# Optimization experiments

Measured on AMD Instinct MI355X. Metric: run time of the kernel, lower is better.

## Reference

```python
import jax, jax.numpy as jnp
import numpy as np

NUM_HEADS = 12
HEAD_DIM = 64
HIDDEN = NUM_HEADS * HEAD_DIM  # 768


def setup_inputs() -> dict:
    key = jax.random.key(0)
    ks = jax.random.split(key, 18)
    B, Ni, Nt, H = 8, 1024, 512, HIDDEN
    inp = {
        "hidden_states": jax.random.normal(ks[0], (B, Ni, H), jnp.float32),
        "text": jax.random.normal(ks[1], (B, Nt, H), jnp.float32),
    }
    names = ["Wq", "Wk", "Wv", "Wqt", "Wkt", "Wvt", "Wo"]
    for i, n in enumerate(names):
        inp[n] = jax.random.normal(ks[2 + i], (H, H), jnp.float32) * 0.02
        inp["b" + n[1:]] = jnp.zeros((H,), jnp.float32)
    return inp


def _split_heads(x):
    # [B, S, H] -> [B, h, S, dh]
    B, S, _ = x.shape
    return x.reshape(B, S, NUM_HEADS, HEAD_DIM).transpose(0, 2, 1, 3)


def _merge_heads(x):
    # [B, h, S, dh] -> [B, S, H]
    B, h, S, dh = x.shape
    return x.transpose(0, 2, 1, 3).reshape(B, S, h * dh)


def _attend(q, k, v):
    scale = 1.0 / jnp.sqrt(jnp.asarray(HEAD_DIM, q.dtype))
    scores = jnp.einsum("bhqd,bhkd->bhqk", q, k) * scale
    probs = jax.nn.softmax(scores, axis=-1)
    ctx = jnp.einsum("bhqk,bhkd->bhqd", probs, v)
    return ctx, probs


def reference(hidden_states, text, Wq, bq, Wk, bk, Wv, bv,
              Wqt, bqt, Wkt, bkt, Wvt, bvt, Wo, bo):
    q_i = _split_heads(hidden_states @ Wq + bq)
    k_i = _split_heads(hidden_states @ Wk + bk)
    v_i = _split_heads(hidden_states @ Wv + bv)
    q_t = _split_heads(text @ Wqt + bqt)
    k_t = _split_heads(text @ Wkt + bkt)
    v_t = _split_heads(text @ Wvt + bvt)

    ctx_ii, weights = _attend(q_i, k_i, v_i)   # img -> img (weights returned, vis=True)
    ctx_tt, _ = _attend(q_t, k_t, v_t)         # text -> text
    ctx_it, _ = _attend(q_i, k_t, v_t)         # img queries, text keys/values
    ctx_ti, _ = _attend(q_t, k_i, v_i)         # text queries, img keys/values

    out_img = (_merge_heads(ctx_ii) + _merge_heads(ctx_it)) * 0.5 @ Wo + bo
    out_text = (_merge_heads(ctx_tt) + _merge_heads(ctx_ti)) * 0.5 @ Wo + bo
    return out_img, out_text, weights
```

## Files before the change

kernel.cpp:

```cpp
#include <hip/hip_runtime.h>

typedef __attribute__((ext_vector_type(4))) float f32x4;
typedef __attribute__((ext_vector_type(8))) short short8;
typedef __attribute__((ext_vector_type(4))) short s16x4;
typedef __attribute__((ext_vector_type(4))) unsigned short us4;
typedef unsigned short u16;
typedef unsigned char uchar;

__device__ __forceinline__ u16 f2b(float f) {
  union { float f; unsigned u; } a; a.f = f;
  unsigned r = a.u + 0x7fffu + ((a.u >> 16) & 1u);
  return (u16)(r >> 16);
}
__device__ __forceinline__ unsigned cvtpk2(float lo, float hi) {
  unsigned r;
  asm("v_cvt_pk_bf16_f32 %0, %1, %2" : "=v"(r) : "v"(lo), "v"(hi));
  return r;
}
__device__ __forceinline__ short8 cvt8(f32x4 a, f32x4 b) {
  union { unsigned u[4]; short8 s; } r;
  r.u[0] = cvtpk2(a[0], a[1]); r.u[1] = cvtpk2(a[2], a[3]);
  r.u[2] = cvtpk2(b[0], b[1]); r.u[3] = cvtpk2(b[2], b[3]);
  return r.s;
}
#define SWZ(r, byteoff) ((((r) * 128) + (byteoff)) ^ (((r) & 7) << 4))

typedef __attribute__((address_space(1))) const void* gp1;
typedef __attribute__((address_space(3))) void* lp3;
__device__ __forceinline__ void gload16(const void* g, void* lds_wave_uniform_base) {
  __builtin_amdgcn_global_load_lds((gp1)g, (lp3)lds_wave_uniform_base, 16, 0, 0);
}

__global__ __launch_bounds__(256) void prep_kernel(
    const float* w0, const float* w1, const float* w2, const float* w3,
    const float* w4, const float* w5, const float* w6, u16* wt,
    const float* __restrict__ h, const float* __restrict__ tx, u16* __restrict__ xb)
{
  const int bid = blockIdx.x, t = threadIdx.x;
  if (bid < 1008) {
    __shared__ float tile[64][65];
    const float* Ws[7] = {w0, w1, w2, w3, w4, w5, w6};
    int z = bid / 144, rem = bid % 144;
    const float* W = Ws[z];
    u16* out = wt + (size_t)z * 589824;
    const int r0 = (rem / 12) * 64, c0 = (rem % 12) * 64;
#pragma unroll
    for (int i = 0; i < 4; ++i) {
      int idx = i * 256 + t;
      int r = idx >> 4, c = (idx & 15) * 4;
      f32x4 v = *(const f32x4*)(W + (size_t)(r0 + r) * 768 + (c0 + c));
      tile[r][c + 0] = v[0]; tile[r][c + 1] = v[1];
      tile[r][c + 2] = v[2]; tile[r][c + 3] = v[3];
    }
    __syncthreads();
#pragma unroll
    for (int i = 0; i < 4; ++i) {
      int idx = i * 256 + t;
      int rn = idx >> 4, c = (idx & 15) * 4;
      union { us4 o; unsigned u[2]; } o;
      o.u[0] = cvtpk2(tile[c + 0][rn], tile[c + 1][rn]);
      o.u[1] = cvtpk2(tile[c + 2][rn], tile[c + 3][rn]);
      *(us4*)(out + (size_t)(c0 + rn) * 768 + (r0 + c)) = o.o;
    }
  } else {
    size_t e = ((size_t)(bid - 1008) * 256 + t) * 8;
    const float* src; size_t off;
    if (e < 6291456) { src = h; off = e; } else { src = tx; off = e - 6291456; }
    f32x4 v0 = *(const f32x4*)(src + off), v1 = *(const f32x4*)(src + off + 4);
    *(short8*)(xb + e) = cvt8(v0, v1);
  }
}

__global__ __launch_bounds__(256) void proj_kernel(
    const u16* __restrict__ Xb, const u16* __restrict__ wt,
    const float* __restrict__ bq, const float* __restrict__ bk, const float* __restrict__ bv,
    const float* __restrict__ bqt, const float* __restrict__ bkt, const float* __restrict__ bvt,
    u16* __restrict__ qi, u16* __restrict__ ki, u16* __restrict__ vti,
    u16* __restrict__ qt, u16* __restrict__ ktx, u16* __restrict__ vtt)
{
  const int bid = blockIdx.x;
  const int wk = (bid & 7) * 216 + (bid >> 3);
  const bool img = wk < 1152;
  const int id = img ? wk : wk - 1152;
  const int y = img ? (id >> 6) : (id >> 5);
  const int x = img ? (id & 63) : (id & 31);
  const int z = y / 6, n0 = (y % 6) * 128, m0 = x * 128;
  const int S = img ? 1024 : 512, logS = img ? 10 : 9;
  const u16* X = img ? Xb : Xb + 6291456;
  const u16* Wt = wt + (img ? 0 : (size_t)3 * 589824) + (size_t)y * 98304;
  const float* bias = img ? (z == 0 ? bq : z == 1 ? bk : bv)
                          : (z == 0 ? bqt : z == 1 ? bkt : bvt);
  u16* out = img ? (z == 0 ? qi : z == 1 ? ki : vti)
                 : (z == 0 ? qt : z == 1 ? ktx : vtt);
  const bool vmode = (z == 2);
  __shared__ unsigned char sm[36864];
  unsigned char* Asm = sm;
  unsigned char* Bsm = sm + 16384;
  const int t = threadIdx.x, w = t >> 6, l = t & 63;
  const int wm = (w & 1) * 64, wn = (w >> 1) * 64;
  f32x4 acc[4][4] = {};
  for (int k0 = 0; k0 < 768; k0 += 64) {
#pragma unroll
    for (int j = 0; j < 4; ++j) {
      int chunk = j * 4 + w;
      int r = chunk * 8 + (l >> 3);
      int cb = ((l & 7) * 16) ^ ((r & 7) << 4);
      gload16(X + (size_t)(m0 + r) * 768 + k0 + cb / 2, Asm + chunk * 1024);
    }
#pragma unroll
    for (int j = 0; j < 4; ++j) {
      int chunk = j * 4 + w;
      int r = chunk * 8 + (l >> 3);
      int cb = ((l & 7) * 16) ^ ((r & 7) << 4);
      gload16(Wt + (size_t)r * 768 + k0 + cb / 2, Bsm + chunk * 1024);
    }
    __syncthreads();
#pragma unroll
    for (int kc = 0; kc < 2; ++kc) {
      short8 af[4], bfr[4];
      const int koff = (kc * 32 + (l >> 4) * 8) * 2;
#pragma unroll
      for (int ms = 0; ms < 4; ++ms) {
        int row = wm + ms * 16 + (l & 15);
        af[ms] = *(const short8*)(Asm + SWZ(row, koff));
      }
#pragma unroll
      for (int ns = 0; ns < 4; ++ns) {
        int row = wn + ns * 16 + (l & 15);
        bfr[ns] = *(const short8*)(Bsm + SWZ(row, koff));
      }
      __builtin_amdgcn_s_setprio(1);
#pragma unroll
      for (int ms = 0; ms < 4; ++ms)
#pragma unroll
        for (int ns = 0; ns < 4; ++ns)
          acc[ms][ns] = __builtin_amdgcn_mfma_f32_16x16x32_bf16(af[ms], bfr[ns], acc[ms][ns], 0, 0, 0);
      __builtin_amdgcn_s_setprio(0);
    }
    __syncthreads();
  }
  float bvv[4];
#pragma unroll
  for (int ns = 0; ns < 4; ++ns) bvv[ns] = bias[n0 + wn + ns * 16 + (l & 15)];
#pragma unroll
  for (int ms = 0; ms < 4; ++ms)
#pragma unroll
    for (int ns = 0; ns < 4; ++ns)
#pragma unroll
      for (int i = 0; i < 4; ++i) {
        u16 u = f2b(acc[ms][ns][i] + bvv[ns]);
        int mm = wm + ms * 16 + (l >> 4) * 4 + i;
        int nn = wn + ns * 16 + (l & 15);
        int row = vmode ? nn : mm, col = vmode ? mm : nn;
        *(u16*)(sm + row * 272 + col * 2) = u;
      }
  __syncthreads();
  if (!vmode) {
#pragma unroll
    for (int i = 0; i < 8; ++i) {
      int idx = i * 256 + t;
      int r = idx >> 4, c = (idx & 15) * 8;
      short8 v = *(const short8*)(sm + r * 272 + c * 2);
      int sg = m0 + r, b = sg >> logS, s = sg & (S - 1);
      int n = n0 + c, hh = n >> 6, d = n & 63;
      *(short8*)(out + (((size_t)b * 12 + hh) * S + s) * 64 + d) = v;
    }
  } else {
#pragma unroll
    for (int i = 0; i < 8; ++i) {
      int idx = i * 256 + t;
      int r = idx >> 4, c = (idx & 15) * 8;
      short8 v = *(const short8*)(sm + r * 272 + c * 2);
      int n = n0 + r, hh = n >> 6, d = n & 63;
      int sg = m0 + c, b = sg >> logS, s = sg & (S - 1);
      *(short8*)(out + (((size_t)b * 12 + hh) * 64 + d) * S + s) = v;
    }
  }
}

__device__ __forceinline__ void stage_k(const u16* Kp, int kt, uchar* Ksm, int w, int l) {
#pragma unroll
  for (int j = 0; j < 2; ++j) {
    int chunk = j * 4 + w;
    int r = chunk * 8 + (l >> 3);
    int cb = ((l & 7) * 16) ^ ((r & 7) << 4);
    gload16(Kp + (size_t)(kt * 64 + r) * 64 + cb / 2, Ksm + chunk * 1024);
  }
}
__device__ __forceinline__ void stage_v(const u16* Vp, int kt, int Sk, uchar* Vsm, int w, int l) {
#pragma unroll
  for (int j = 0; j < 2; ++j) {
    int chunk = j * 4 + w;
    int r = chunk * 8 + (l >> 3);
    int cb = ((l & 7) * 16) ^ ((r & 7) << 4);
    gload16(Vp + (size_t)r * Sk + kt * 64 + cb / 2, Vsm + chunk * 1024);
  }
}
__device__ __forceinline__ void kfrags(const uchar* Ksm, int l, short8 kf[8]) {
#pragma unroll
  for (int kc = 0; kc < 2; ++kc)
#pragma unroll
    for (int sub = 0; sub < 4; ++sub) {
      int row = sub * 16 + (l & 15);
      kf[kc * 4 + sub] = *(const short8*)(Ksm + SWZ(row, (kc * 32 + (l >> 4) * 8) * 2));
    }
}
__device__ __forceinline__ void qk_swapped(const short8 qf[2][2], const short8 kf[8], f32x4 sfr[2][4]) {
  __builtin_amdgcn_s_setprio(1);
#pragma unroll
  for (int m = 0; m < 2; ++m)
#pragma unroll
    for (int kc = 0; kc < 2; ++kc)
#pragma unroll
      for (int sub = 0; sub < 4; ++sub)
        sfr[m][sub] = __builtin_amdgcn_mfma_f32_16x16x32_bf16(kf[kc * 4 + sub], qf[m][kc], sfr[m][sub], 0, 0, 0);
  __builtin_amdgcn_s_setprio(0);
}
__device__ __forceinline__ void vfrags_sigma(const uchar* Vsm, int l, short8 vb[8]) {
#pragma unroll
  for (int kc = 0; kc < 2; ++kc)
#pragma unroll
    for (int ds = 0; ds < 4; ++ds) {
      int row = ds * 16 + (l & 15);
      union { s16x4 h[2]; short8 s; } u;
      u.h[0] = *(const s16x4*)(Vsm + SWZ(row, 64 * kc + 8 * (l >> 4)));
      u.h[1] = *(const s16x4*)(Vsm + SWZ(row, 64 * kc + 32 + 8 * (l >> 4)));
      vb[kc * 4 + ds] = u.s;
    }
}
__device__ __forceinline__ void pa_sigma(const float ps[16], short8 pa[2]) {
#pragma unroll
  for (int kc = 0; kc < 2; ++kc) {
    union { unsigned u[4]; short8 s; } r;
    r.u[0] = cvtpk2(ps[8 * kc + 0], ps[8 * kc + 1]);
    r.u[1] = cvtpk2(ps[8 * kc + 2], ps[8 * kc + 3]);
    r.u[2] = cvtpk2(ps[8 * kc + 4], ps[8 * kc + 5]);
    r.u[3] = cvtpk2(ps[8 * kc + 6], ps[8 * kc + 7]);
    pa[kc] = r.s;
  }
}
__device__ __forceinline__ void pv_sigma(const short8 pa[2], const short8 vb[8], f32x4 og[4]) {
  __builtin_amdgcn_s_setprio(1);
#pragma unroll
  for (int kc = 0; kc < 2; ++kc)
#pragma unroll
    for (int ds = 0; ds < 4; ++ds)
      og[ds] = __builtin_amdgcn_mfma_f32_16x16x32_bf16(pa[kc], vb[kc * 4 + ds], og[ds], 0, 0, 0);
  __builtin_amdgcn_s_setprio(0);
}
__device__ __forceinline__ void pass_unnorm(
    const u16* __restrict__ Kp, const u16* __restrict__ Vp, int Sk,
    const short8 qf[2][2], uchar* Ks0, uchar* Ks1, uchar* Vs0, uchar* Vs1,
    int w, int l, f32x4 og[2][4], float ll[2])
{
  const int nkt = Sk >> 6;
  stage_k(Kp, 0, Ks0, w, l);
  stage_v(Vp, 0, Sk, Vs0, w, l);
  __syncthreads();
  for (int kt = 0; kt < nkt; ++kt) {
    uchar* Kc = (kt & 1) ? Ks1 : Ks0;
    uchar* Vc = (kt & 1) ? Vs1 : Vs0;
    if (kt + 1 < nkt) {
      stage_k(Kp, kt + 1, (kt & 1) ? Ks0 : Ks1, w, l);
      stage_v(Vp, kt + 1, Sk, (kt & 1) ? Vs0 : Vs1, w, l);
    }
    short8 kf[8];
    kfrags(Kc, l, kf);
    f32x4 sfr[2][4] = {};
    qk_swapped(qf, kf, sfr);
    short8 vb[8];
    vfrags_sigma(Vc, l, vb);
#pragma unroll
    for (int m = 0; m < 2; ++m) {
      float ps[16];
#pragma unroll
      for (int sub = 0; sub < 4; ++sub)
#pragma unroll
        for (int i = 0; i < 4; ++i) {
          float p = __expf(sfr[m][sub][i] * 0.125f);
          ll[m] += p;
          ps[sub * 4 + i] = p;
        }
      short8 pa[2];
      pa_sigma(ps, pa);
      pv_sigma(pa, vb, og[m]);
    }
    __syncthreads();
  }
}

__global__ __launch_bounds__(256) void attn_kernel(
    const u16* __restrict__ qi, const u16* __restrict__ ki, const u16* __restrict__ vti,
    const u16* __restrict__ qt, const u16* __restrict__ ktx, const u16* __restrict__ vtt,
    u16* __restrict__ cimg, u16* __restrict__ ctxt, float* __restrict__ weights)
{
  __shared__ uchar smem[50176];
  const int t = threadIdx.x, w = t >> 6, l = t & 63;
  uchar* Ks0 = smem;
  uchar* Ks1 = smem + 8192;
  uchar* Vs0 = smem + 16384;
  uchar* Vs1 = smem + 24576;
  uchar* Pf  = smem + 32768 + w * 4352;

  const int bid = blockIdx.x;
  const int wk = (bid & 7) * 144 + (bid >> 3);
  const bool img = wk < 768;
  const int id = img ? wk : wk - 768;
  const int x = img ? (id & 7) : (id & 3);
  const int head = img ? (id >> 3) : (id >> 2);
  const int b = head / 12, h = head % 12;
  const int Sq = img ? 1024 : 512;
  const int SkA = img ? 1024 : 512, SkB = img ? 512 : 1024;
  const u16* Qp = (img ? qi : qt) + (size_t)head * Sq * 64;
  const u16* KpA = (img ? ki : ktx) + (size_t)head * SkA * 64;
  const u16* VpA = (img ? vti : vtt) + (size_t)head * 64 * SkA;
  const u16* KpB = (img ? ktx : ki) + (size_t)head * SkB * 64;
  const u16* VpB = (img ? vtt : vti) + (size_t)head * 64 * SkB;
  u16* CTX = img ? cimg : ctxt;
  float* PROBS = img ? weights : nullptr;
  const int q0 = x * 128;

  short8 qf[2][2];
#pragma unroll
  for (int m = 0; m < 2; ++m) {
    int row = q0 + m * 64 + w * 16 + (l & 15);
    qf[m][0] = *(const short8*)(Qp + (size_t)row * 64 + (l >> 4) * 8);
    qf[m][1] = *(const short8*)(Qp + (size_t)row * 64 + 32 + (l >> 4) * 8);
  }

  f32x4 of[2][4] = {};
  if (PROBS) {
    float ll[2] = {0.f, 0.f};
    const int nkt = SkA >> 6;
    stage_k(KpA, 0, Ks0, w, l);
    __syncthreads();
    for (int kt = 0; kt < nkt; ++kt) {
      uchar* Kc = (kt & 1) ? Ks1 : Ks0;
      if (kt + 1 < nkt) stage_k(KpA, kt + 1, (kt & 1) ? Ks0 : Ks1, w, l);
      short8 kf[8];
      kfrags(Kc, l, kf);
      f32x4 sfr[2][4] = {};
      qk_swapped(qf, kf, sfr);
#pragma unroll
      for (int m = 0; m < 2; ++m)
#pragma unroll
        for (int sub = 0; sub < 4; ++sub)
#pragma unroll
          for (int i = 0; i < 4; ++i) ll[m] += __expf(sfr[m][sub][i] * 0.125f);
      __syncthreads();
    }
    stage_k(KpA, 0, Ks0, w, l);
    stage_v(VpA, 0, SkA, Vs0, w, l);
    float rl[2];
#pragma unroll
    for (int m = 0; m < 2; ++m) {
      ll[m] += __shfl_xor(ll[m], 16);
      ll[m] += __shfl_xor(ll[m], 32);
      rl[m] = 1.0f / ll[m];
    }
    __syncthreads();
    for (int kt = 0; kt < nkt; ++kt) {
      uchar* Kc = (kt & 1) ? Ks1 : Ks0;
      uchar* Vc = (kt & 1) ? Vs1 : Vs0;
      if (kt + 1 < nkt) {
        stage_k(KpA, kt + 1, (kt & 1) ? Ks0 : Ks1, w, l);
        stage_v(VpA, kt + 1, SkA, (kt & 1) ? Vs0 : Vs1, w, l);
      }
      short8 kf[8];
      kfrags(Kc, l, kf);
      f32x4 sfr[2][4] = {};
      qk_swapped(qf, kf, sfr);
      short8 vb[8];
      vfrags_sigma(Vc, l, vb);
#pragma unroll
      for (int m = 0; m < 2; ++m) {
        float ps[16];
#pragma unroll
        for (int sub = 0; sub < 4; ++sub) {
#pragma unroll
          for (int i = 0; i < 4; ++i)
            ps[sub * 4 + i] = __expf(sfr[m][sub][i] * 0.125f) * rl[m];
          *(f32x4*)(Pf + (l & 15) * 272 + (sub * 16 + (l >> 4) * 4) * 4) =
              *(const f32x4*)&ps[sub * 4];
        }
        const size_t pbase = ((size_t)head * Sq + q0 + m * 64 + w * 16);
#pragma unroll
        for (int psr = 0; psr < 4; ++psr) {
          int row = psr * 4 + (l >> 4);
          f32x4 v = *(const f32x4*)(Pf + row * 272 + (l & 15) * 16);
          *(f32x4*)(PROBS + (pbase + row) * (size_t)SkA + kt * 64 + (l & 15) * 4) = v;
        }
        short8 pa[2];
        pa_sigma(ps, pa);
        pv_sigma(pa, vb, of[m]);
      }
      __syncthreads();
    }
#pragma unroll
    for (int m = 0; m < 2; ++m)
#pragma unroll
      for (int ds = 0; ds < 4; ++ds) of[m][ds] *= 0.5f;
  } else {
    float ll[2] = {0.f, 0.f};
    pass_unnorm(KpA, VpA, SkA, qf, Ks0, Ks1, Vs0, Vs1, w, l, of, ll);
#pragma unroll
    for (int m = 0; m < 2; ++m) {
      ll[m] += __shfl_xor(ll[m], 16);
      ll[m] += __shfl_xor(ll[m], 32);
      float r = 0.5f / ll[m];
#pragma unroll
      for (int i = 0; i < 4; ++i) {
        float lv = __int_as_float(__builtin_amdgcn_ds_bpermute(
            ((l >> 4) * 4 + i) * 4, __float_as_int(r)));
#pragma unroll
        for (int ds = 0; ds < 4; ++ds) of[m][ds][i] *= lv;
      }
    }
  }
  {
    f32x4 og[2][4] = {};
    float l2[2] = {0.f, 0.f};
    pass_unnorm(KpB, VpB, SkB, qf, Ks0, Ks1, Vs0, Vs1, w, l, og, l2);
#pragma unroll
    for (int m = 0; m < 2; ++m) {
      l2[m] += __shfl_xor(l2[m], 16);
      l2[m] += __shfl_xor(l2[m], 32);
      float r = 0.5f / l2[m];
#pragma unroll
      for (int i = 0; i < 4; ++i) {
        float lv = __int_as_float(__builtin_amdgcn_ds_bpermute(
            ((l >> 4) * 4 + i) * 4, __float_as_int(r)));
#pragma unroll
        for (int ds = 0; ds < 4; ++ds) of[m][ds][i] += og[m][ds][i] * lv;
      }
    }
  }
#pragma unroll
  for (int m = 0; m < 2; ++m) {
#pragma unroll
    for (int ds = 0; ds < 4; ++ds)
#pragma unroll
      for (int i = 0; i < 4; ++i)
        *(float*)(Pf + ((l >> 4) * 4 + i) * 272 + (ds * 16 + (l & 15)) * 4) = of[m][ds][i];
#pragma unroll
    for (int i = 0; i < 2; ++i) {
      int it = i * 64 + l;
      int r = it >> 3, cg = it & 7;
      f32x4 v0 = *(const f32x4*)(Pf + r * 272 + cg * 32);
      f32x4 v1 = *(const f32x4*)(Pf + r * 272 + cg * 32 + 16);
      int s = q0 + m * 64 + w * 16 + r;
      *(short8*)(CTX + ((size_t)b * Sq + s) * 768 + h * 64 + cg * 8) = cvt8(v0, v1);
    }
  }
}

__global__ __launch_bounds__(256) void outproj_kernel(
    const u16* __restrict__ cimg, const u16* __restrict__ ctxt,
    const u16* __restrict__ Wto, const float* __restrict__ bias,
    float* __restrict__ out_img, float* __restrict__ out_text)
{
  const int bid = blockIdx.x;
  const int wk = (bid & 7) * 72 + (bid >> 3);
  const bool img = wk < 384;
  const int id = img ? wk : wk - 384;
  const int y = img ? (id >> 6) : (id >> 5);
  const int x = img ? (id & 63) : (id & 31);
  const u16* C = img ? cimg : ctxt;
  float* OUT = img ? out_img : out_text;
  const int m0 = x * 128, n0 = y * 128;
  __shared__ unsigned char sm[32768];
  unsigned char* Asm = sm;
  unsigned char* Bsm = sm + 16384;
  const int t = threadIdx.x, w = t >> 6, l = t & 63;
  const int wm = (w & 1) * 64, wn = (w >> 1) * 64;
  f32x4 acc[4][4] = {};
  for (int k0 = 0; k0 < 768; k0 += 64) {
#pragma unroll
    for (int j = 0; j < 4; ++j) {
      int chunk = j * 4 + w;
      int r = chunk * 8 + (l >> 3);
      int cb = ((l & 7) * 16) ^ ((r & 7) << 4);
      gload16(C + (size_t)(m0 + r) * 768 + k0 + cb / 2, Asm + chunk * 1024);
    }
#pragma unroll
    for (int j = 0; j < 4; ++j) {
      int chunk = j * 4 + w;
      int r = chunk * 8 + (l >> 3);
      int cb = ((l & 7) * 16) ^ ((r & 7) << 4);
      gload16(Wto + (size_t)(n0 + r) * 768 + k0 + cb / 2, Bsm + chunk * 1024);
    }
    __syncthreads();
#pragma unroll
    for (int kc = 0; kc < 2; ++kc) {
      short8 af[4], bfr[4];
      const int koff = (kc * 32 + (l >> 4) * 8) * 2;
#pragma unroll
      for (int ms = 0; ms < 4; ++ms) {
        int row = wm + ms * 16 + (l & 15);
        af[ms] = *(const short8*)(Asm + SWZ(row, koff));
      }
#pragma unroll
      for (int ns = 0; ns < 4; ++ns) {
        int row = wn + ns * 16 + (l & 15);
        bfr[ns] = *(const short8*)(Bsm + SWZ(row, koff));
      }
      __builtin_amdgcn_s_setprio(1);
#pragma unroll
      for (int ms = 0; ms < 4; ++ms)
#pragma unroll
        for (int ns = 0; ns < 4; ++ns)
          acc[ms][ns] = __builtin_amdgcn_mfma_f32_16x16x32_bf16(af[ms], bfr[ns], acc[ms][ns], 0, 0, 0);
      __builtin_amdgcn_s_setprio(0);
    }
    __syncthreads();
  }
#pragma unroll
  for (int ms = 0; ms < 4; ++ms)
#pragma unroll
    for (int ns = 0; ns < 4; ++ns) {
      float bv = bias[n0 + wn + ns * 16 + (l & 15)];
#pragma unroll
      for (int i = 0; i < 4; ++i) {
        int mm = m0 + wm + ms * 16 + (l >> 4) * 4 + i;
        int nn = n0 + wn + ns * 16 + (l & 15);
        OUT[(size_t)mm * 768 + nn] = acc[ms][ns][i] + bv;
      }
    }
}

extern "C" void kernel_launch(void* const* d_in, const int* in_sizes, int n_in,
                              void* d_out, int out_size, void* d_ws, size_t ws_size,
                              hipStream_t stream)
{
  const float* hidden = (const float*)d_in[0];
  const float* text   = (const float*)d_in[1];
  const float* Wq  = (const float*)d_in[2];  const float* bq  = (const float*)d_in[3];
  const float* Wk  = (const float*)d_in[4];  const float* bk  = (const float*)d_in[5];
  const float* Wv  = (const float*)d_in[6];  const float* bv  = (const float*)d_in[7];
  const float* Wqt = (const float*)d_in[8];  const float* bqt = (const float*)d_in[9];
  const float* Wkt = (const float*)d_in[10]; const float* bkt = (const float*)d_in[11];
  const float* Wvt = (const float*)d_in[12]; const float* bvt = (const float*)d_in[13];
  const float* Wo  = (const float*)d_in[14]; const float* bo  = (const float*)d_in[15];

  u16* wt   = (u16*)d_ws;
  u16* xb   = wt + 7 * 589824;
  u16* qi   = xb + 9437184;
  u16* ki   = qi + 6291456;
  u16* vti  = ki + 6291456;
  u16* qt   = vti + 6291456;
  u16* ktx  = qt + 3145728;
  u16* vtt  = ktx + 3145728;
  u16* cimg = vtt + 3145728;
  u16* ctxt = cimg + 6291456;

  float* out_img  = (float*)d_out;
  float* out_text = out_img + 6291456;
  float* weights  = out_text + 3145728;

  prep_kernel<<<5616, 256, 0, stream>>>(Wq, Wk, Wv, Wqt, Wkt, Wvt, Wo, wt,
                                        hidden, text, xb);
  proj_kernel<<<1728, 256, 0, stream>>>(xb, wt, bq, bk, bv, bqt, bkt, bvt,
                                        qi, ki, vti, qt, ktx, vtt);
  attn_kernel<<<1152, 256, 0, stream>>>(qi, ki, vti, qt, ktx, vtt,
                                        cimg, ctxt, weights);
  outproj_kernel<<<576, 256, 0, stream>>>(cimg, ctxt, wt + 6 * 589824, bo,
                                          out_img, out_text);
}
```

Baseline: 366.7 us.

## Use 8 waves per attention block, one 16-row query tile per wave

The attention kernel moves from 4 waves each owning two 16-row query tiles to 8 waves each owning one, with 512-thread blocks and launch bounds requesting 4 blocks per CU. Each wave now stages one K/V chunk per tile, and the probability writes go straight from registers to global memory instead of being transposed through shared memory. The context output is staged in shared memory as bf16, which shrinks shared memory to 32 KB. The intent is higher occupancy, less register pressure and less LDS traffic. In exchange, the probability stores are less coalesced and there are more waves per barrier.

```diff
diff --git a/kernel.cpp b/kernel.cpp
--- a/kernel.cpp
+++ b/kernel.cpp
@@ -178,23 +178,15 @@
   }
 }
 
-__device__ __forceinline__ void stage_k(const u16* Kp, int kt, uchar* Ksm, int w, int l) {
-#pragma unroll
-  for (int j = 0; j < 2; ++j) {
-    int chunk = j * 4 + w;
-    int r = chunk * 8 + (l >> 3);
-    int cb = ((l & 7) * 16) ^ ((r & 7) << 4);
-    gload16(Kp + (size_t)(kt * 64 + r) * 64 + cb / 2, Ksm + chunk * 1024);
-  }
-}
-__device__ __forceinline__ void stage_v(const u16* Vp, int kt, int Sk, uchar* Vsm, int w, int l) {
-#pragma unroll
-  for (int j = 0; j < 2; ++j) {
-    int chunk = j * 4 + w;
-    int r = chunk * 8 + (l >> 3);
-    int cb = ((l & 7) * 16) ^ ((r & 7) << 4);
-    gload16(Vp + (size_t)r * Sk + kt * 64 + cb / 2, Vsm + chunk * 1024);
-  }
+__device__ __forceinline__ void stage_k8(const u16* Kp, int kt, uchar* Ksm, int w, int l) {
+  int r = w * 8 + (l >> 3);
+  int cb = ((l & 7) * 16) ^ ((r & 7) << 4);
+  gload16(Kp + (size_t)(kt * 64 + r) * 64 + cb / 2, Ksm + w * 1024);
+}
+__device__ __forceinline__ void stage_v8(const u16* Vp, int kt, int Sk, uchar* Vsm, int w, int l) {
+  int r = w * 8 + (l >> 3);
+  int cb = ((l & 7) * 16) ^ ((r & 7) << 4);
+  gload16(Vp + (size_t)r * Sk + kt * 64 + cb / 2, Vsm + w * 1024);
 }
 __device__ __forceinline__ void kfrags(const uchar* Ksm, int l, short8 kf[8]) {
 #pragma unroll
@@ -205,15 +197,13 @@
       kf[kc * 4 + sub] = *(const short8*)(Ksm + SWZ(row, (kc * 32 + (l >> 4) * 8) * 2));
     }
 }
-__device__ __forceinline__ void qk_swapped(const short8 qf[2][2], const short8 kf[8], f32x4 sfr[2][4]) {
+__device__ __forceinline__ void qk_swapped(const short8 qf[2], const short8 kf[8], f32x4 sfr[4]) {
   __builtin_amdgcn_s_setprio(1);
 #pragma unroll
-  for (int m = 0; m < 2; ++m)
-#pragma unroll
-    for (int kc = 0; kc < 2; ++kc)
-#pragma unroll
-      for (int sub = 0; sub < 4; ++sub)
-        sfr[m][sub] = __builtin_amdgcn_mfma_f32_16x16x32_bf16(kf[kc * 4 + sub], qf[m][kc], sfr[m][sub], 0, 0, 0);
+  for (int kc = 0; kc < 2; ++kc)
+#pragma unroll
+    for (int sub = 0; sub < 4; ++sub)
+      sfr[sub] = __builtin_amdgcn_mfma_f32_16x16x32_bf16(kf[kc * 4 + sub], qf[kc], sfr[sub], 0, 0, 0);
   __builtin_amdgcn_s_setprio(0);
 }
 __device__ __forceinline__ void vfrags_sigma(const uchar* Vsm, int l, short8 vb[8]) {
@@ -250,57 +240,53 @@
 }
 __device__ __forceinline__ void pass_unnorm(
     const u16* __restrict__ Kp, const u16* __restrict__ Vp, int Sk,
-    const short8 qf[2][2], uchar* Ks0, uchar* Ks1, uchar* Vs0, uchar* Vs1,
-    int w, int l, f32x4 og[2][4], float ll[2])
+    const short8 qf[2], uchar* Ks0, uchar* Ks1, uchar* Vs0, uchar* Vs1,
+    int w, int l, f32x4 og[4], float& ll)
 {
   const int nkt = Sk >> 6;
-  stage_k(Kp, 0, Ks0, w, l);
-  stage_v(Vp, 0, Sk, Vs0, w, l);
+  stage_k8(Kp, 0, Ks0, w, l);
+  stage_v8(Vp, 0, Sk, Vs0, w, l);
   __syncthreads();
   for (int kt = 0; kt < nkt; ++kt) {
     uchar* Kc = (kt & 1) ? Ks1 : Ks0;
     uchar* Vc = (kt & 1) ? Vs1 : Vs0;
     if (kt + 1 < nkt) {
-      stage_k(Kp, kt + 1, (kt & 1) ? Ks0 : Ks1, w, l);
-      stage_v(Vp, kt + 1, Sk, (kt & 1) ? Vs0 : Vs1, w, l);
+      stage_k8(Kp, kt + 1, (kt & 1) ? Ks0 : Ks1, w, l);
+      stage_v8(Vp, kt + 1, Sk, (kt & 1) ? Vs0 : Vs1, w, l);
     }
     short8 kf[8];
     kfrags(Kc, l, kf);
-    f32x4 sfr[2][4] = {};
+    f32x4 sfr[4] = {};
     qk_swapped(qf, kf, sfr);
+    float ps[16];
+#pragma unroll
+    for (int sub = 0; sub < 4; ++sub)
+#pragma unroll
+      for (int i = 0; i < 4; ++i) {
+        float p = __expf(sfr[sub][i] * 0.125f);
+        ll += p;
+        ps[sub * 4 + i] = p;
+      }
+    short8 pa[2];
+    pa_sigma(ps, pa);
     short8 vb[8];
     vfrags_sigma(Vc, l, vb);
-#pragma unroll
-    for (int m = 0; m < 2; ++m) {
-      float ps[16];
-#pragma unroll
-      for (int sub = 0; sub < 4; ++sub)
-#pragma unroll
-        for (int i = 0; i < 4; ++i) {
-          float p = __expf(sfr[m][sub][i] * 0.125f);
-          ll[m] += p;
-          ps[sub * 4 + i] = p;
-        }
-      short8 pa[2];
-      pa_sigma(ps, pa);
-      pv_sigma(pa, vb, og[m]);
-    }
-    __syncthreads();
-  }
-}
-
-__global__ __launch_bounds__(256) void attn_kernel(
+    pv_sigma(pa, vb, og);
+    __syncthreads();
+  }
+}
+
+__global__ __launch_bounds__(512, 4) void attn_kernel(
     const u16* __restrict__ qi, const u16* __restrict__ ki, const u16* __restrict__ vti,
     const u16* __restrict__ qt, const u16* __restrict__ ktx, const u16* __restrict__ vtt,
     u16* __restrict__ cimg, u16* __restrict__ ctxt, float* __restrict__ weights)
 {
-  __shared__ uchar smem[50176];
+  __shared__ uchar smem[32768];
   const int t = threadIdx.x, w = t >> 6, l = t & 63;
   uchar* Ks0 = smem;
   uchar* Ks1 = smem + 8192;
   uchar* Vs0 = smem + 16384;
   uchar* Vs1 = smem + 24576;
-  uchar* Pf  = smem + 32768 + w * 4352;
 
   const int bid = blockIdx.x;
   const int wk = (bid & 7) * 144 + (bid >> 3);
@@ -319,137 +305,110 @@
   u16* CTX = img ? cimg : ctxt;
   float* PROBS = img ? weights : nullptr;
   const int q0 = x * 128;
-
-  short8 qf[2][2];
-#pragma unroll
-  for (int m = 0; m < 2; ++m) {
-    int row = q0 + m * 64 + w * 16 + (l & 15);
-    qf[m][0] = *(const short8*)(Qp + (size_t)row * 64 + (l >> 4) * 8);
-    qf[m][1] = *(const short8*)(Qp + (size_t)row * 64 + 32 + (l >> 4) * 8);
-  }
-
-  f32x4 of[2][4] = {};
+  const int qrow = q0 + w * 16 + (l & 15);
+
+  short8 qf[2];
+  qf[0] = *(const short8*)(Qp + (size_t)qrow * 64 + (l >> 4) * 8);
+  qf[1] = *(const short8*)(Qp + (size_t)qrow * 64 + 32 + (l >> 4) * 8);
+
+  f32x4 of[4] = {};
   if (PROBS) {
-    float ll[2] = {0.f, 0.f};
+    float ll = 0.f;
     const int nkt = SkA >> 6;
-    stage_k(KpA, 0, Ks0, w, l);
+    stage_k8(KpA, 0, Ks0, w, l);
     __syncthreads();
     for (int kt = 0; kt < nkt; ++kt) {
       uchar* Kc = (kt & 1) ? Ks1 : Ks0;
-      if (kt + 1 < nkt) stage_k(KpA, kt + 1, (kt & 1) ? Ks0 : Ks1, w, l);
+      if (kt + 1 < nkt) stage_k8(KpA, kt + 1, (kt & 1) ? Ks0 : Ks1, w, l);
       short8 kf[8];
       kfrags(Kc, l, kf);
-      f32x4 sfr[2][4] = {};
+      f32x4 sfr[4] = {};
       qk_swapped(qf, kf, sfr);
 #pragma unroll
-      for (int m = 0; m < 2; ++m)
-#pragma unroll
-        for (int sub = 0; sub < 4; ++sub)
-#pragma unroll
-          for (int i = 0; i < 4; ++i) ll[m] += __expf(sfr[m][sub][i] * 0.125f);
+      for (int sub = 0; sub < 4; ++sub)
+#pragma unroll
+        for (int i = 0; i < 4; ++i) ll += __expf(sfr[sub][i] * 0.125f);
       __syncthreads();
     }
-    stage_k(KpA, 0, Ks0, w, l);
-    stage_v(VpA, 0, SkA, Vs0, w, l);
-    float rl[2];
-#pragma unroll
-    for (int m = 0; m < 2; ++m) {
-      ll[m] += __shfl_xor(ll[m], 16);
-      ll[m] += __shfl_xor(ll[m], 32);
-      rl[m] = 1.0f / ll[m];
-    }
-    __syncthreads();
+    stage_k8(KpA, 0, Ks0, w, l);
+    stage_v8(VpA, 0, SkA, Vs0, w, l);
+    ll += __shfl_xor(ll, 16);
+    ll += __shfl_xor(ll, 32);
+    float rl = 1.0f / ll;
+    __syncthreads();
+    float* prow = PROBS + ((size_t)head * Sq + qrow) * SkA;
     for (int kt = 0; kt < nkt; ++kt) {
       uchar* Kc = (kt & 1) ? Ks1 : Ks0;
       uchar* Vc = (kt & 1) ? Vs1 : Vs0;
       if (kt + 1 < nkt) {
-        stage_k(KpA, kt + 1, (kt & 1) ? Ks0 : Ks1, w, l);
-        stage_v(VpA, kt + 1, SkA, (kt & 1) ? Vs0 : Vs1, w, l);
+        stage_k8(KpA, kt + 1, (kt & 1) ? Ks0 : Ks1, w, l);
+        stage_v8(VpA, kt + 1, SkA, (kt & 1) ? Vs0 : Vs1, w, l);
       }
       short8 kf[8];
       kfrags(Kc, l, kf);
-      f32x4 sfr[2][4] = {};
+      f32x4 sfr[4] = {};
       qk_swapped(qf, kf, sfr);
+      float ps[16];
+#pragma unroll
+      for (int sub = 0; sub < 4; ++sub) {
+#pragma unroll
+        for (int i = 0; i < 4; ++i)
+          ps[sub * 4 + i] = __expf(sfr[sub][i] * 0.125f) * rl;
+        *(f32x4*)(prow + kt * 64 + sub * 16 + (l >> 4) * 4) = *(const f32x4*)&ps[sub * 4];
+      }
+      short8 pa[2];
+      pa_sigma(ps, pa);
       short8 vb[8];
       vfrags_sigma(Vc, l, vb);
-#pragma unroll
-      for (int m = 0; m < 2; ++m) {
-        float ps[16];
-#pragma unroll
-        for (int sub = 0; sub < 4; ++sub) {
-#pragma unroll
-          for (int i = 0; i < 4; ++i)
-            ps[sub * 4 + i] = __expf(sfr[m][sub][i] * 0.125f) * rl[m];
-          *(f32x4*)(Pf + (l & 15) * 272 + (sub * 16 + (l >> 4) * 4) * 4) =
-              *(const f32x4*)&ps[sub * 4];
-        }
-        const size_t pbase = ((size_t)head * Sq + q0 + m * 64 + w * 16);
-#pragma unroll
-        for (int psr = 0; psr < 4; ++psr) {
-          int row = psr * 4 + (l >> 4);
-          f32x4 v = *(const f32x4*)(Pf + row * 272 + (l & 15) * 16);
-          *(f32x4*)(PROBS + (pbase + row) * (size_t)SkA + kt * 64 + (l & 15) * 4) = v;
-        }
-        short8 pa[2];
-        pa_sigma(ps, pa);
-        pv_sigma(pa, vb, of[m]);
-      }
+      pv_sigma(pa, vb, of);
       __syncthreads();
     }
 #pragma unroll
-    for (int m = 0; m < 2; ++m)
-#pragma unroll
-      for (int ds = 0; ds < 4; ++ds) of[m][ds] *= 0.5f;
+    for (int ds = 0; ds < 4; ++ds) of[ds] *= 0.5f;
   } else {
-    float ll[2] = {0.f, 0.f};
+    float ll = 0.f;
     pass_unnorm(KpA, VpA, SkA, qf, Ks0, Ks1, Vs0, Vs1, w, l, of, ll);
-#pragma unroll
-    for (int m = 0; m < 2; ++m) {
-      ll[m] += __shfl_xor(ll[m], 16);
-      ll[m] += __shfl_xor(ll[m], 32);
-      float r = 0.5f / ll[m];
-#pragma unroll
-      for (int i = 0; i < 4; ++i) {
-        float lv = __int_as_float(__builtin_amdgcn_ds_bpermute(
-            ((l >> 4) * 4 + i) * 4, __float_as_int(r)));
-#pragma unroll
-        for (int ds = 0; ds < 4; ++ds) of[m][ds][i] *= lv;
-      }
+    ll += __shfl_xor(ll, 16);
+    ll += __shfl_xor(ll, 32);
+    float r = 0.5f / ll;
+#pragma unroll
+    for (int i = 0; i < 4; ++i) {
+      float lv = __int_as_float(__builtin_amdgcn_ds_bpermute(
+          ((l >> 4) * 4 + i) * 4, __float_as_int(r)));
+#pragma unroll
+      for (int ds = 0; ds < 4; ++ds) of[ds][i] *= lv;
     }
   }
   {
-    f32x4 og[2][4] = {};
-    float l2[2] = {0.f, 0.f};
+    f32x4 og[4] = {};
+    float l2 = 0.f;
     pass_unnorm(KpB, VpB, SkB, qf, Ks0, Ks1, Vs0, Vs1, w, l, og, l2);
-#pragma unroll
-    for (int m = 0; m < 2; ++m) {
-      l2[m] += __shfl_xor(l2[m], 16);
-      l2[m] += __shfl_xor(l2[m], 32);
-      float r = 0.5f / l2[m];
-#pragma unroll
-      for (int i = 0; i < 4; ++i) {
-        float lv = __int_as_float(__builtin_amdgcn_ds_bpermute(
-            ((l >> 4) * 4 + i) * 4, __float_as_int(r)));
-#pragma unroll
-        for (int ds = 0; ds < 4; ++ds) of[m][ds][i] += og[m][ds][i] * lv;
-      }
-    }
-  }
-#pragma unroll
-  for (int m = 0; m < 2; ++m) {
+    l2 += __shfl_xor(l2, 16);
+    l2 += __shfl_xor(l2, 32);
+    float r = 0.5f / l2;
+#pragma unroll
+    for (int i = 0; i < 4; ++i) {
+      float lv = __int_as_float(__builtin_amdgcn_ds_bpermute(
+          ((l >> 4) * 4 + i) * 4, __float_as_int(r)));
+#pragma unroll
+      for (int ds = 0; ds < 4; ++ds) of[ds][i] += og[ds][i] * lv;
+    }
+  }
+  __syncthreads();
+  {
+    uchar* Wb = smem + w * 2176;
 #pragma unroll
     for (int ds = 0; ds < 4; ++ds)
 #pragma unroll
       for (int i = 0; i < 4; ++i)
-        *(float*)(Pf + ((l >> 4) * 4 + i) * 272 + (ds * 16 + (l & 15)) * 4) = of[m][ds][i];
+        *(u16*)(Wb + ((l >> 4) * 4 + i) * 136 + (16 * ds + (l & 15)) * 2) = f2b(of[ds][i]);
 #pragma unroll
     for (int i = 0; i < 2; ++i) {
       int it = i * 64 + l;
       int r = it >> 3, cg = it & 7;
-      f32x4 v0 = *(const f32x4*)(Pf + r * 272 + cg * 32);
-      f32x4 v1 = *(const f32x4*)(Pf + r * 272 + cg * 32 + 16);
-      int s = q0 + m * 64 + w * 16 + r;
-      *(short8*)(CTX + ((size_t)b * Sq + s) * 768 + h * 64 + cg * 8) = cvt8(v0, v1);
+      short8 v = *(const short8*)(Wb + r * 136 + cg * 16);
+      int s = q0 + w * 16 + r;
+      *(short8*)(CTX + ((size_t)b * Sq + s) * 768 + h * 64 + cg * 8) = v;
     }
   }
 }
@@ -561,7 +520,7 @@
                                         hidden, text, xb);
   proj_kernel<<<1728, 256, 0, stream>>>(xb, wt, bq, bk, bv, bqt, bkt, bvt,
                                         qi, ki, vti, qt, ktx, vtt);
-  attn_kernel<<<1152, 256, 0, stream>>>(qi, ki, vti, qt, ktx, vtt,
+  attn_kernel<<<1152, 512, 0, stream>>>(qi, ki, vti, qt, ktx, vtt,
                                         cimg, ctxt, weights);
   outproj_kernel<<<576, 256, 0, stream>>>(cimg, ctxt, wt + 6 * 589824, bo,
                                           out_img, out_text);
```

Result: faster. 324.8 us (-11.4%).
